# Kernel tuning notes

Hardware: AMD Instinct MI355X
Metric: run time of the kernel (lower is better)

## Reference

```python
import jax, jax.numpy as jnp
import numpy as np

N_NODES = 100000
N_EDGES = 1600000
DIM_IN = 64
DIM_OUT = 40
K_HOPS = 3


def setup_inputs() -> dict:
    key = jax.random.key(0)
    ks = jax.random.split(key, 6)
    x = jax.random.normal(ks[0], (N_NODES, DIM_IN), dtype=jnp.float32)
    edge_index = jax.random.randint(ks[1], (2, N_EDGES), 0, N_NODES, dtype=jnp.int64)
    W_sgc = jax.random.normal(ks[2], (DIM_IN, DIM_IN), dtype=jnp.float32) * (1.0 / np.sqrt(DIM_IN))
    b_sgc = jax.random.normal(ks[3], (DIM_IN,), dtype=jnp.float32) * 0.02
    W_head = jax.random.normal(ks[4], (DIM_IN, DIM_OUT), dtype=jnp.float32) * (1.0 / np.sqrt(DIM_IN))
    b_head = jax.random.normal(ks[5], (DIM_OUT,), dtype=jnp.float32) * 0.02
    return {"x": x, "edge_index": edge_index, "W_sgc": W_sgc, "b_sgc": b_sgc,
            "W_head": W_head, "b_head": b_head}


def _sgc_forward(x, src, dst, norm, W_sgc, b_sgc, W_head, b_head):
    n = x.shape[0]
    # K-hop normalized adjacency propagation: x <- A_hat @ x, K times
    for _ in range(K_HOPS):
        x = jax.ops.segment_sum(norm[:, None] * x[src], dst, num_segments=n)
    # SGConv linear projection
    x = x @ W_sgc + b_sgc
    # dropout is identity at inference (training=False)
    # post-MP node head: Linear(dim_in -> dim_out)
    return x @ W_head + b_head


def reference(x, edge_index, W_sgc, b_sgc, W_head, b_head):
    n = x.shape[0]
    # gcn_norm with self-loops (PyG SGConv default):
    loop = jnp.arange(n, dtype=edge_index.dtype)
    src = jnp.concatenate([edge_index[0], loop])  # message source j
    dst = jnp.concatenate([edge_index[1], loop])  # message target i
    ew = jnp.ones(src.shape[0], dtype=x.dtype)
    deg = jax.ops.segment_sum(ew, dst, num_segments=n)
    dinv = jnp.where(deg > 0, jax.lax.rsqrt(deg), 0.0)
    norm = dinv[src] * dinv[dst]  # [E + N]
    return _sgc_forward(x, src, dst, norm, W_sgc, b_sgc, W_head, b_head)
```

## Files before the change

### kernel.cpp

```cpp
#include <hip/hip_runtime.h>
#include <hip/hip_bf16.h>
#include <hip/hip_fp16.h>

#define DIMI 64
#define DIMO 40
#define PADO 64

#define NBK_SHIFT 9
#define NPBK 512
#define NBKMAX 256
#define BCAP 9216
#define CHUNK 4096


__global__ void k_zero(int* __restrict__ p, int n) {
    int i = blockIdx.x * blockDim.x + threadIdx.x;
    if (i < n) p[i] = 0;
}

__global__ void k_binA(const int* __restrict__ src, const int* __restrict__ dst,
                       int* __restrict__ bcnt, int2* __restrict__ ebDS,
                       int E, int nbk) {
    __shared__ int h[NBKMAX];
    __shared__ int lb[NBKMAX];
    __shared__ int lc[NBKMAX];
    __shared__ int gb[NBKMAX];
    __shared__ int2 eb[CHUNK];
    int t = threadIdx.x;
    int e0 = blockIdx.x * CHUNK;
    int e1 = min(e0 + CHUNK, E);
    int nE = e1 - e0;
    h[t] = 0;
    __syncthreads();
    int d[CHUNK / 256], s[CHUNK / 256];
    #pragma unroll
    for (int u = 0; u < CHUNK / 256; u++) {
        int idx = e0 + t + u * 256;
        if (idx < e1) {
            d[u] = dst[idx];
            s[u] = src[idx];
            atomicAdd(&h[d[u] >> NBK_SHIFT], 1);
        }
    }
    __syncthreads();
    int orig = h[t];
    for (int o = 1; o < 256; o <<= 1) {
        int v = (t >= o) ? h[t - o] : 0;
        __syncthreads();
        h[t] += v;
        __syncthreads();
    }
    lb[t] = h[t] - orig;
    lc[t] = 0;
    gb[t] = orig ? atomicAdd(&bcnt[t], orig) : 0;
    __syncthreads();
    #pragma unroll
    for (int u = 0; u < CHUNK / 256; u++) {
        int idx = e0 + t + u * 256;
        if (idx < e1) {
            int b = d[u] >> NBK_SHIFT;
            int r = atomicAdd(&lc[b], 1);
            eb[lb[b] + r] = make_int2(d[u], s[u]);
        }
    }
    __syncthreads();
    for (int i = t; i < nE; i += 256) {
        int2 e = eb[i];
        int b = e.x >> NBK_SHIFT;
        int slot = gb[b] + (i - lb[b]);
        if (slot < BCAP) ebDS[(size_t)b * BCAP + slot] = e;
    }
}

__global__ void k_binB(const int* __restrict__ bcnt, const int2* __restrict__ ebDS,
                       int* __restrict__ counts, int N) {
    __shared__ int lh[NPBK];
    int b = blockIdx.x, t = threadIdx.x;
    for (int j = t; j < NPBK; j += 256) lh[j] = 0;
    __syncthreads();
    int n = min(bcnt[b], BCAP);
    size_t base = (size_t)b * BCAP;
    for (int i = t; i < n; i += 256)
        atomicAdd(&lh[ebDS[base + i].x & (NPBK - 1)], 1);
    __syncthreads();
    int d0 = b << NBK_SHIFT;
    for (int j = t; j < NPBK; j += 256) {
        int dd = d0 + j;
        if (dd < N) counts[dd] = lh[j];
    }
}

__global__ void k_binC(const int* __restrict__ bcnt, const int2* __restrict__ ebDS,
                       const int* __restrict__ off, int* __restrict__ col,
                       int N, int E) {
    __shared__ int loff[NPBK];
    __shared__ int lc[NPBK];
    __shared__ int scol[BCAP];
    int b = blockIdx.x, t = threadIdx.x;
    int d0 = b << NBK_SHIFT;
    for (int j = t; j < NPBK; j += 256) {
        int dd = d0 + j;
        loff[j] = (dd < N) ? off[dd] : E;
        lc[j] = 0;
    }
    __syncthreads();
    int n = min(bcnt[b], BCAP);
    size_t base = (size_t)b * BCAP;
    int o0 = loff[0];
    for (int i = t; i < n; i += 256) {
        int2 e = ebDS[base + i];
        int local = e.x & (NPBK - 1);
        int r = atomicAdd(&lc[local], 1);
        int idx = loff[local] - o0 + r;
        if (idx < BCAP) scol[idx] = e.y;
    }
    __syncthreads();
    for (int i = t; i < n; i += 256) col[o0 + i] = scol[i];
}


__global__ void k_hist(const int* __restrict__ dst, int* __restrict__ counts, int E) {
    int i = blockIdx.x * blockDim.x + threadIdx.x;
    if (i < E) atomicAdd(&counts[dst[i]], 1);
}

__global__ void k_scatter(const int* __restrict__ src, const int* __restrict__ dst,
                          const int* __restrict__ off, int* __restrict__ cursor,
                          int* __restrict__ col, int E) {
    int i = blockIdx.x * blockDim.x + threadIdx.x;
    if (i < E) {
        int d = dst[i];
        int p = off[d] + atomicAdd(&cursor[d], 1);
        col[p] = src[i];
    }
}


__global__ void k_block_sums(const int* __restrict__ counts, int* __restrict__ partial, int n) {
    __shared__ int s[256];
    int i = blockIdx.x * 256 + threadIdx.x;
    s[threadIdx.x] = (i < n) ? counts[i] : 0;
    __syncthreads();
    for (int st = 128; st > 0; st >>= 1) {
        if (threadIdx.x < st) s[threadIdx.x] += s[threadIdx.x + st];
        __syncthreads();
    }
    if (threadIdx.x == 0) partial[blockIdx.x] = s[0];
}

__global__ void k_scan_partials(int* partial, int nb) {
    __shared__ int s[1024];
    int t = threadIdx.x;
    int orig = (t < nb) ? partial[t] : 0;
    s[t] = orig;
    __syncthreads();
    for (int o = 1; o < 1024; o <<= 1) {
        int v = (t >= o) ? s[t - o] : 0;
        __syncthreads();
        s[t] += v;
        __syncthreads();
    }
    if (t < nb) partial[t] = s[t] - orig;
}

__global__ void k_scan_final(const int* __restrict__ counts, const int* __restrict__ partial,
                             int* __restrict__ off, float* __restrict__ dinv, int n) {
    __shared__ int s[256];
    int t = threadIdx.x;
    int i = blockIdx.x * 256 + t;
    int orig = (i < n) ? counts[i] : 0;
    s[t] = orig;
    __syncthreads();
    for (int o = 1; o < 256; o <<= 1) {
        int v = (t >= o) ? s[t - o] : 0;
        __syncthreads();
        s[t] += v;
        __syncthreads();
    }
    if (i < n) {
        off[i] = s[t] - orig + partial[blockIdx.x];
        dinv[i] = rsqrtf((float)(orig + 1));
    }
}


__global__ void k_wc(const float* __restrict__ Wsgc, const float* __restrict__ bsgc,
                     const float* __restrict__ Whead, const float* __restrict__ bhead,
                     float* __restrict__ Wc, float* __restrict__ bc) {
    __shared__ float sA[DIMI * DIMI];
    __shared__ float sB[DIMI * DIMO];
    int t = threadIdx.x;
    for (int i = t; i < DIMI * DIMI; i += 256) sA[i] = Wsgc[i];
    for (int i = t; i < DIMI * DIMO; i += 256) sB[i] = Whead[i];
    __syncthreads();
    for (int o = t; o < DIMI * DIMO; o += 256) {
        int k = o / DIMO, j = o % DIMO;
        float acc = 0.f;
        #pragma unroll
        for (int m = 0; m < DIMI; m++) acc += sA[k * DIMI + m] * sB[m * DIMO + j];
        Wc[o] = acc;
    }
    if (t < DIMO) {
        float acc = bhead[t];
        #pragma unroll
        for (int m = 0; m < DIMI; m++) acc += bsgc[m] * sB[m * DIMO + t];
        bc[t] = acc;
    }
}

__global__ void k_proj(const float* __restrict__ x, const float* __restrict__ Wc,
                       const float* __restrict__ dinv, __half* __restrict__ y, int N) {
    __shared__ float sX[32 * DIMI];
    __shared__ float sW[DIMI * DIMO];
    int t = threadIdx.x;
    int n0 = blockIdx.x * 32;
    for (int i = t; i < DIMI * DIMO; i += 256) sW[i] = Wc[i];
    const float4* x4 = (const float4*)x;
    float4* sX4 = (float4*)sX;
    for (int i = t; i < 32 * (DIMI / 4); i += 256) {
        int r = n0 + i / (DIMI / 4);
        sX4[i] = (r < N) ? x4[(long)r * (DIMI / 4) + (i & (DIMI / 4 - 1))]
                         : make_float4(0.f, 0.f, 0.f, 0.f);
    }
    __syncthreads();
    for (int o = t; o < 32 * DIMO; o += 256) {
        int li = o / DIMO, j = o % DIMO;
        int node = n0 + li;
        if (node < N) {
            float acc = 0.f;
            #pragma unroll
            for (int k = 0; k < DIMI; k++) acc += sX[li * DIMI + k] * sW[k * DIMO + j];
            y[(long)node * PADO + j] = __float2half(dinv[node] * acc);
        }
    }
}

__global__ void k_hop(const __half* __restrict__ xin, __half* __restrict__ xoutH,
                      float* __restrict__ outF,
                      const int* __restrict__ off, const int* __restrict__ counts,
                      const float* __restrict__ dinv,
                      const int* __restrict__ col,
                      const float* __restrict__ bc, int finalHop, int N) {
    int gtid = blockIdx.x * blockDim.x + threadIdx.x;
    int node = gtid >> 6;
    int lane = threadIdx.x & 63;
    if (node >= N) return;
    int l = lane < DIMO ? lane : DIMO - 1;
    int rs = off[node];
    int cnt = counts[node];
    int cidx = (lane < cnt) ? col[rs + lane] : node;
    float acc = __half2float(xin[(long)node * PADO + l]);
    int cmain = cnt < 64 ? cnt : 64;
    int e = 0;
    for (; e + 16 <= cmain; e += 16) {
        float v[16];
        #pragma unroll
        for (int u = 0; u < 16; u++) {
            int c = __shfl(cidx, e + u, 64);
            v[u] = __half2float(xin[(long)c * PADO + l]);
        }
        float s01 = (v[0] + v[1]) + (v[2] + v[3]);
        float s23 = (v[4] + v[5]) + (v[6] + v[7]);
        float s45 = (v[8] + v[9]) + (v[10] + v[11]);
        float s67 = (v[12] + v[13]) + (v[14] + v[15]);
        acc += (s01 + s23) + (s45 + s67);
    }
    for (; e + 4 <= cmain; e += 4) {
        float v[4];
        #pragma unroll
        for (int u = 0; u < 4; u++) {
            int c = __shfl(cidx, e + u, 64);
            v[u] = __half2float(xin[(long)c * PADO + l]);
        }
        acc += (v[0] + v[1]) + (v[2] + v[3]);
    }
    for (; e < cmain; e++) {
        int c = __shfl(cidx, e, 64);
        acc += __half2float(xin[(long)c * PADO + l]);
    }
    for (int e2 = 64; e2 < cnt; e2++) {
        acc += __half2float(xin[(long)col[rs + e2] * PADO + l]);
    }
    float di = dinv[node];
    float scale = finalHop ? di : di * di;
    if (lane < DIMO) {
        float r = scale * acc;
        if (finalHop) outF[(long)node * DIMO + lane] = r + bc[lane];
        else xoutH[(long)node * PADO + lane] = __float2half(r);
    }
}


extern "C" void kernel_launch(void* const* d_in, const int* in_sizes, int n_in,
                              void* d_out, int out_size, void* d_ws, size_t ws_size,
                              hipStream_t stream) {
    const float* x     = (const float*)d_in[0];
    const int*   ei    = (const int*)d_in[1];
    const float* Wsgc  = (const float*)d_in[2];
    const float* bsgc  = (const float*)d_in[3];
    const float* Whead = (const float*)d_in[4];
    const float* bhead = (const float*)d_in[5];
    float* out = (float*)d_out;

    const int N = in_sizes[0] / DIMI;
    const int E = in_sizes[1] / 2;
    const int* src = ei;
    const int* dst = ei + E;
    const int nbk = (N + NPBK - 1) >> NBK_SHIFT;

    char* w = (char*)d_ws;
    auto carve = [&](size_t bytes) {
        char* p = w;
        w += (bytes + 255) & ~(size_t)255;
        return p;
    };
    int*   counts  = (int*)  carve((size_t)N * 4);
    int*   cursor  = (int*)  carve((size_t)N * 4);
    int*   off     = (int*)  carve((size_t)N * 4);
    float* dinv    = (float*)carve((size_t)N * 4);
    int*   partial = (int*)  carve(1024 * 4);
    int*   col     = (int*)  carve((size_t)E * 4);
    float* Wc      = (float*)carve(DIMI * DIMO * 4);
    float* bc      = (float*)carve(DIMO * 4);
    int*   bcnt    = (int*)  carve((size_t)nbk * 4);
    size_t xbytes  = (size_t)N * PADO * 2;
    size_t ebytes  = (size_t)nbk * BCAP * 8;
    size_t ubytes  = ebytes > 2 * xbytes ? ebytes : 2 * xbytes;
    char*  uni     = carve(ubytes);
    int2*   ebDS = (int2*)uni;
    __half* xA   = (__half*)uni;
    __half* xB   = (__half*)(uni + xbytes);
    size_t total_need = (size_t)(w - (char*)d_ws);
    const bool useBuckets = (ws_size >= total_need) && (nbk <= NBKMAX);

    const int B = 256;
    int nbN = (N + B - 1) / B;
    int nbE = (E + B - 1) / B;

    if (useBuckets) {
        k_zero<<<(nbk + B - 1) / B, B, 0, stream>>>(bcnt, nbk);
        int nbA = (E + CHUNK - 1) / CHUNK;
        k_binA<<<nbA, B, 0, stream>>>(src, dst, bcnt, ebDS, E, nbk);
        k_binB<<<nbk, B, 0, stream>>>(bcnt, ebDS, counts, N);
        k_block_sums<<<nbN, B, 0, stream>>>(counts, partial, N);
        k_scan_partials<<<1, 1024, 0, stream>>>(partial, nbN);
        k_scan_final<<<nbN, B, 0, stream>>>(counts, partial, off, dinv, N);
        k_binC<<<nbk, B, 0, stream>>>(bcnt, ebDS, off, col, N, E);
    } else {
        k_zero<<<nbN, B, 0, stream>>>(counts, N);
        k_zero<<<nbN, B, 0, stream>>>(cursor, N);
        k_hist<<<nbE, B, 0, stream>>>(dst, counts, E);
        k_block_sums<<<nbN, B, 0, stream>>>(counts, partial, N);
        k_scan_partials<<<1, 1024, 0, stream>>>(partial, nbN);
        k_scan_final<<<nbN, B, 0, stream>>>(counts, partial, off, dinv, N);
        k_scatter<<<nbE, B, 0, stream>>>(src, dst, off, cursor, col, E);
    }

    k_wc<<<1, 256, 0, stream>>>(Wsgc, bsgc, Whead, bhead, Wc, bc);
    k_proj<<<(N + 31) / 32, 256, 0, stream>>>(x, Wc, dinv, xA, N);

    int hopBlocks = (N * 64 + B - 1) / B;
    k_hop<<<hopBlocks, B, 0, stream>>>(xA, xB, out, off, counts, dinv, col, bc, 0, N);
    k_hop<<<hopBlocks, B, 0, stream>>>(xB, xA, out, off, counts, dinv, col, bc, 0, N);
    k_hop<<<hopBlocks, B, 0, stream>>>(xA, xB, out, off, counts, dinv, col, bc, 1, N);
}
```

Measured before the change: 252.8 us.

## Split hop features into 32+8 half arrays and fuse bucket CSR build

Node features were stored as 64 padded halves per row even though only 40 are used. They are now split into a 32-wide and an 8-wide array, so each gathered row touches 64+16 bytes instead of a 128-byte padded row. Separately, the CSR build replaces the binB / block_sums / scan_partials / scan_final / binC sequence with a scan over bucket counts plus one fused kernel. That kernel computes counts, offsets, dinv and the column order per bucket, cutting several launches and global passes. The split layout adds a per-lane branch on which base pointer to use and needs two memory segments per gathered row.

```diff
diff --git a/kernel.cpp b/kernel.cpp
--- a/kernel.cpp
+++ b/kernel.cpp
@@ -4,7 +4,8 @@
 
 #define DIMI 64
 #define DIMO 40
-#define PADO 64
+#define DLO  32
+#define DHI  8
 
 #define NBK_SHIFT 9
 #define NPBK 512
@@ -72,50 +73,72 @@
     }
 }
 
-__global__ void k_binB(const int* __restrict__ bcnt, const int2* __restrict__ ebDS,
-                       int* __restrict__ counts, int N) {
-    __shared__ int lh[NPBK];
+__global__ void k_scan_bcnt(const int* __restrict__ bcnt, int* __restrict__ bbase, int nbk) {
+    __shared__ int s[256];
+    int t = threadIdx.x;
+    int orig = (t < nbk) ? min(bcnt[t], BCAP) : 0;
+    s[t] = orig;
+    __syncthreads();
+    for (int o = 1; o < 256; o <<= 1) {
+        int v = (t >= o) ? s[t - o] : 0;
+        __syncthreads();
+        s[t] += v;
+        __syncthreads();
+    }
+    if (t < nbk) bbase[t] = s[t] - orig;
+}
+
+__global__ void k_binBC(const int* __restrict__ bcnt, const int* __restrict__ bbase,
+                        const int2* __restrict__ ebDS,
+                        int* __restrict__ counts, int* __restrict__ off,
+                        float* __restrict__ dinv, int* __restrict__ col,
+                        int N) {
+    __shared__ int sh[NPBK];
+    __shared__ int so[NPBK];
+    __shared__ int slc[NPBK];
+    __shared__ int scol[BCAP];
     int b = blockIdx.x, t = threadIdx.x;
-    for (int j = t; j < NPBK; j += 256) lh[j] = 0;
+    sh[t] = 0; sh[t + 256] = 0;
     __syncthreads();
     int n = min(bcnt[b], BCAP);
     size_t base = (size_t)b * BCAP;
     for (int i = t; i < n; i += 256)
-        atomicAdd(&lh[ebDS[base + i].x & (NPBK - 1)], 1);
-    __syncthreads();
+        atomicAdd(&sh[ebDS[base + i].x & (NPBK - 1)], 1);
+    __syncthreads();
+    so[t] = sh[t]; so[t + 256] = sh[t + 256];
+    __syncthreads();
+    for (int o = 1; o < NPBK; o <<= 1) {
+        int v0 = (t >= o) ? sh[t - o] : 0;
+        int v1 = (t + 256 >= o) ? sh[t + 256 - o] : 0;
+        __syncthreads();
+        sh[t] += v0; sh[t + 256] += v1;
+        __syncthreads();
+    }
+    int gbase = bbase[b];
     int d0 = b << NBK_SHIFT;
-    for (int j = t; j < NPBK; j += 256) {
+    #pragma unroll
+    for (int half = 0; half < 2; half++) {
+        int j = t + half * 256;
+        int orig = so[j];
+        int excl = sh[j] - orig;
         int dd = d0 + j;
-        if (dd < N) counts[dd] = lh[j];
-    }
-}
-
-__global__ void k_binC(const int* __restrict__ bcnt, const int2* __restrict__ ebDS,
-                       const int* __restrict__ off, int* __restrict__ col,
-                       int N, int E) {
-    __shared__ int loff[NPBK];
-    __shared__ int lc[NPBK];
-    __shared__ int scol[BCAP];
-    int b = blockIdx.x, t = threadIdx.x;
-    int d0 = b << NBK_SHIFT;
-    for (int j = t; j < NPBK; j += 256) {
-        int dd = d0 + j;
-        loff[j] = (dd < N) ? off[dd] : E;
-        lc[j] = 0;
-    }
-    __syncthreads();
-    int n = min(bcnt[b], BCAP);
-    size_t base = (size_t)b * BCAP;
-    int o0 = loff[0];
+        if (dd < N) {
+            counts[dd] = orig;
+            off[dd] = gbase + excl;
+            dinv[dd] = rsqrtf((float)(orig + 1));
+        }
+        so[j] = excl;
+        slc[j] = 0;
+    }
+    __syncthreads();
     for (int i = t; i < n; i += 256) {
         int2 e = ebDS[base + i];
         int local = e.x & (NPBK - 1);
-        int r = atomicAdd(&lc[local], 1);
-        int idx = loff[local] - o0 + r;
-        if (idx < BCAP) scol[idx] = e.y;
-    }
-    __syncthreads();
-    for (int i = t; i < n; i += 256) col[o0 + i] = scol[i];
+        int r = atomicAdd(&slc[local], 1);
+        scol[so[local] + r] = e.y;
+    }
+    __syncthreads();
+    for (int i = t; i < n; i += 256) col[gbase + i] = scol[i];
 }
 
 
@@ -135,7 +158,6 @@
     }
 }
 
-
 __global__ void k_block_sums(const int* __restrict__ counts, int* __restrict__ partial, int n) {
     __shared__ int s[256];
     int i = blockIdx.x * 256 + threadIdx.x;
@@ -209,7 +231,8 @@
 }
 
 __global__ void k_proj(const float* __restrict__ x, const float* __restrict__ Wc,
-                       const float* __restrict__ dinv, __half* __restrict__ y, int N) {
+                       const float* __restrict__ dinv,
+                       __half* __restrict__ yL, __half* __restrict__ yH, int N) {
     __shared__ float sX[32 * DIMI];
     __shared__ float sW[DIMI * DIMO];
     int t = threadIdx.x;
@@ -230,12 +253,15 @@
             float acc = 0.f;
             #pragma unroll
             for (int k = 0; k < DIMI; k++) acc += sX[li * DIMI + k] * sW[k * DIMO + j];
-            y[(long)node * PADO + j] = __float2half(dinv[node] * acc);
-        }
-    }
-}
-
-__global__ void k_hop(const __half* __restrict__ xin, __half* __restrict__ xoutH,
+            __half v = __float2half(dinv[node] * acc);
+            if (j < DLO) yL[(long)node * DLO + j] = v;
+            else         yH[(long)node * DHI + (j - DLO)] = v;
+        }
+    }
+}
+
+__global__ void k_hop(const __half* __restrict__ xLin, const __half* __restrict__ xHin,
+                      __half* __restrict__ xLout, __half* __restrict__ xHout,
                       float* __restrict__ outF,
                       const int* __restrict__ off, const int* __restrict__ counts,
                       const float* __restrict__ dinv,
@@ -246,10 +272,13 @@
     int lane = threadIdx.x & 63;
     if (node >= N) return;
     int l = lane < DIMO ? lane : DIMO - 1;
+    const __half* base; long stride; int foff;
+    if (l < DLO) { base = xLin; stride = DLO; foff = l; }
+    else         { base = xHin; stride = DHI; foff = l - DLO; }
     int rs = off[node];
     int cnt = counts[node];
     int cidx = (lane < cnt) ? col[rs + lane] : node;
-    float acc = __half2float(xin[(long)node * PADO + l]);
+    float acc = __half2float(base[(long)node * stride + foff]);
     int cmain = cnt < 64 ? cnt : 64;
     int e = 0;
     for (; e + 16 <= cmain; e += 16) {
@@ -257,7 +286,7 @@
         #pragma unroll
         for (int u = 0; u < 16; u++) {
             int c = __shfl(cidx, e + u, 64);
-            v[u] = __half2float(xin[(long)c * PADO + l]);
+            v[u] = __half2float(base[(long)c * stride + foff]);
         }
         float s01 = (v[0] + v[1]) + (v[2] + v[3]);
         float s23 = (v[4] + v[5]) + (v[6] + v[7]);
@@ -270,23 +299,29 @@
         #pragma unroll
         for (int u = 0; u < 4; u++) {
             int c = __shfl(cidx, e + u, 64);
-            v[u] = __half2float(xin[(long)c * PADO + l]);
+            v[u] = __half2float(base[(long)c * stride + foff]);
         }
         acc += (v[0] + v[1]) + (v[2] + v[3]);
     }
     for (; e < cmain; e++) {
         int c = __shfl(cidx, e, 64);
-        acc += __half2float(xin[(long)c * PADO + l]);
+        acc += __half2float(base[(long)c * stride + foff]);
     }
     for (int e2 = 64; e2 < cnt; e2++) {
-        acc += __half2float(xin[(long)col[rs + e2] * PADO + l]);
+        int c = col[rs + e2];
+        acc += __half2float(base[(long)c * stride + foff]);
     }
     float di = dinv[node];
     float scale = finalHop ? di : di * di;
     if (lane < DIMO) {
         float r = scale * acc;
-        if (finalHop) outF[(long)node * DIMO + lane] = r + bc[lane];
-        else xoutH[(long)node * PADO + lane] = __float2half(r);
+        if (finalHop) {
+            outF[(long)node * DIMO + lane] = r + bc[lane];
+        } else {
+            __half h = __float2half(r);
+            if (lane < DLO) xLout[(long)node * DLO + lane] = h;
+            else            xHout[(long)node * DHI + (lane - DLO)] = h;
+        }
     }
 }
 
@@ -323,13 +358,18 @@
     float* Wc      = (float*)carve(DIMI * DIMO * 4);
     float* bc      = (float*)carve(DIMO * 4);
     int*   bcnt    = (int*)  carve((size_t)nbk * 4);
-    size_t xbytes  = (size_t)N * PADO * 2;
+    int*   bbase   = (int*)  carve((size_t)nbk * 4);
+    size_t lbytes  = (size_t)N * DLO * 2;
+    size_t hbytes  = (size_t)N * DHI * 2;
+    size_t xbytes  = lbytes + hbytes;
     size_t ebytes  = (size_t)nbk * BCAP * 8;
     size_t ubytes  = ebytes > 2 * xbytes ? ebytes : 2 * xbytes;
     char*  uni     = carve(ubytes);
     int2*   ebDS = (int2*)uni;
-    __half* xA   = (__half*)uni;
-    __half* xB   = (__half*)(uni + xbytes);
+    __half* xLA  = (__half*)uni;
+    __half* xHA  = (__half*)(uni + lbytes);
+    __half* xLB  = (__half*)(uni + xbytes);
+    __half* xHB  = (__half*)(uni + xbytes + lbytes);
     size_t total_need = (size_t)(w - (char*)d_ws);
     const bool useBuckets = (ws_size >= total_need) && (nbk <= NBKMAX);
 
@@ -341,11 +381,8 @@
         k_zero<<<(nbk + B - 1) / B, B, 0, stream>>>(bcnt, nbk);
         int nbA = (E + CHUNK - 1) / CHUNK;
         k_binA<<<nbA, B, 0, stream>>>(src, dst, bcnt, ebDS, E, nbk);
-        k_binB<<<nbk, B, 0, stream>>>(bcnt, ebDS, counts, N);
-        k_block_sums<<<nbN, B, 0, stream>>>(counts, partial, N);
-        k_scan_partials<<<1, 1024, 0, stream>>>(partial, nbN);
-        k_scan_final<<<nbN, B, 0, stream>>>(counts, partial, off, dinv, N);
-        k_binC<<<nbk, B, 0, stream>>>(bcnt, ebDS, off, col, N, E);
+        k_scan_bcnt<<<1, 256, 0, stream>>>(bcnt, bbase, nbk);
+        k_binBC<<<nbk, B, 0, stream>>>(bcnt, bbase, ebDS, counts, off, dinv, col, N);
     } else {
         k_zero<<<nbN, B, 0, stream>>>(counts, N);
         k_zero<<<nbN, B, 0, stream>>>(cursor, N);
@@ -357,10 +394,10 @@
     }
 
     k_wc<<<1, 256, 0, stream>>>(Wsgc, bsgc, Whead, bhead, Wc, bc);
-    k_proj<<<(N + 31) / 32, 256, 0, stream>>>(x, Wc, dinv, xA, N);
+    k_proj<<<(N + 31) / 32, 256, 0, stream>>>(x, Wc, dinv, xLA, xHA, N);
 
     int hopBlocks = (N * 64 + B - 1) / B;
-    k_hop<<<hopBlocks, B, 0, stream>>>(xA, xB, out, off, counts, dinv, col, bc, 0, N);
-    k_hop<<<hopBlocks, B, 0, stream>>>(xB, xA, out, off, counts, dinv, col, bc, 0, N);
-    k_hop<<<hopBlocks, B, 0, stream>>>(xA, xB, out, off, counts, dinv, col, bc, 1, N);
-}
+    k_hop<<<hopBlocks, B, 0, stream>>>(xLA, xHA, xLB, xHB, out, off, counts, dinv, col, bc, 0, N);
+    k_hop<<<hopBlocks, B, 0, stream>>>(xLB, xHB, xLA, xHA, out, off, counts, dinv, col, bc, 0, N);
+    k_hop<<<hopBlocks, B, 0, stream>>>(xLA, xHA, xLB, xHB, out, off, counts, dinv, col, bc, 1, N);
+}
```

Measured after the change: 248.8 us. No clear change (-1.6%).
